# Optimization experiments

Measured on AMD Instinct MI355X. Metric: run time of the kernel, lower is better.

## Reference

```python
import jax, jax.numpy as jnp
import numpy as np

NUM_HEADS = 4
NUM_LEVELS = 4
NUM_POINTS = 8
EMBED = 256
HEAD_DIM = EMBED // NUM_HEADS
SHAPES = np.array([[92, 160], [46, 80], [23, 40], [12, 20]], dtype=np.int64)  # (h, w) per level
NUM_VALUE = int((SHAPES[:, 0] * SHAPES[:, 1]).sum())  # 19560
DEPTH = 64
NQ = 20000
BS = 1
NZ = 4  # num_Z_anchors; NUM_POINTS % NZ == 0


def _depth_bias():
    # replicates init_smpl_off_weights for sampling_offsets_depth.bias
    th = np.arange(NUM_HEADS) * (2.0 * np.pi / NUM_HEADS)
    g = ((np.cos(th) + np.sin(th)) / 2.0)[:, None, None] * np.ones((NUM_HEADS, NUM_LEVELS, NUM_POINTS))
    g = g * (np.arange(NUM_POINTS) + 1)[None, None, :]
    return jnp.asarray(g.reshape(-1), dtype=jnp.float32)


def setup_inputs() -> dict:
    key = jax.random.key(0)
    ks = jax.random.split(key, 8)
    f = jnp.float32
    s = 0.02
    query = jax.random.normal(ks[0], (BS, NQ, EMBED), f)
    value = jax.random.normal(ks[1], (BS, NUM_VALUE, EMBED), f)
    value_dpt_dist = jax.nn.softmax(jax.random.normal(ks[2], (BS, NUM_VALUE, DEPTH), f), axis=-1)
    reference_points = jax.random.uniform(ks[3], (BS, NQ, NZ, 3), f)
    spatial_shapes = jnp.asarray(SHAPES)
    level_start_index = jnp.asarray(np.concatenate([[0], np.cumsum(SHAPES[:, 0] * SHAPES[:, 1])[:-1]]))
    Wv = jax.random.normal(ks[4], (EMBED, EMBED), f) * s
    bv = jnp.zeros((EMBED,), f)
    Wo = jax.random.normal(ks[5], (EMBED, NUM_HEADS * NUM_LEVELS * NUM_POINTS * 2), f) * s
    bo = jax.random.normal(ks[6], (NUM_HEADS * NUM_LEVELS * NUM_POINTS * 2,), f) * 0.5
    Wod = jnp.zeros((EMBED, NUM_HEADS * NUM_LEVELS * NUM_POINTS), f)  # constant_init 0.0
    bod = _depth_bias()
    Wa = jax.random.normal(ks[7], (EMBED, NUM_HEADS * NUM_LEVELS * NUM_POINTS), f) * s
    ba = jnp.zeros((NUM_HEADS * NUM_LEVELS * NUM_POINTS,), f)
    return dict(query=query, value=value, value_dpt_dist=value_dpt_dist,
                reference_points=reference_points, spatial_shapes=spatial_shapes,
                level_start_index=level_start_index, Wv=Wv, bv=bv, Wo=Wo, bo=bo,
                Wod=Wod, bod=bod, Wa=Wa, ba=ba)


def _forward(query, value, value_dpt_dist, reference_points, spatial_shapes,
             level_start_index, Wv, bv, Wo, bo, Wod, bod, Wa, ba):
    bs, nq, _ = query.shape
    H, L, P = NUM_HEADS, NUM_LEVELS, NUM_POINTS
    dh = HEAD_DIM
    D = value_dpt_dist.shape[-1]
    dt = query.dtype
    shapes = np.asarray(spatial_shapes)  # static level shapes

    v = (value @ Wv + bv).reshape(bs, -1, H, dh)  # value_proj
    off_uv = (query @ Wo + bo).reshape(bs, nq, H, L, P, 2)
    off_d = (query @ Wod + bod).reshape(bs, nq, H, L, P, 1)
    off = jnp.concatenate([off_uv, off_d], axis=-1)  # (bs,nq,H,L,P,3)
    attn = jax.nn.softmax((query @ Wa + ba).reshape(bs, nq, H, L * P), axis=-1)
    attn = attn.reshape(bs, nq, H, L, P)

    # offset_normalizer = (w, h, D) per level
    norm = jnp.asarray(np.stack([shapes[:, 1], shapes[:, 0], np.full(L, D)], -1), dtype=dt)
    off = off / norm[None, None, None, :, None, :]
    Z = reference_points.shape[2]
    off = off.reshape(bs, nq, H, L, P // Z, Z, 3)
    loc = (reference_points[:, :, None, None, None, :, :] + off).reshape(bs, nq, H, L, P, 3)

    starts = np.concatenate([[0], np.cumsum(shapes[:, 0] * shapes[:, 1])]).astype(int)
    gather_bh = jax.vmap(jax.vmap(lambda a, i: a[i]))   # over (bs, heads)
    gather_b = jax.vmap(lambda a, i: a[i])              # over bs

    out = jnp.zeros((bs, nq, H, dh), dt)
    for l in range(L):
        Hl, Wl = int(shapes[l, 0]), int(shapes[l, 1])
        v_l = v[:, starts[l]:starts[l + 1]].transpose(0, 2, 1, 3)          # (bs,H,HW,dh)
        d_l = value_dpt_dist[:, starts[l]:starts[l + 1]].reshape(bs, Hl * Wl * D)
        ll = loc[:, :, :, l]                                               # (bs,nq,H,P,3)
        # grid_sample (align_corners=False) pixel coordinates
        x = ll[..., 0] * Wl - 0.5
        y = ll[..., 1] * Hl - 0.5
        z = ll[..., 2] * D - 0.5
        x0f, y0f, z0f = jnp.floor(x), jnp.floor(y), jnp.floor(z)
        fx, fy, fz = x - x0f, y - y0f, z - z0f
        x0 = x0f.astype(jnp.int32); y0 = y0f.astype(jnp.int32); z0 = z0f.astype(jnp.int32)
        z0c = jnp.clip(z0, 0, D - 1)
        z1c = jnp.clip(z0 + 1, 0, D - 1)
        wz0 = (1.0 - fz) * ((z0 >= 0) & (z0 <= D - 1)).astype(dt)
        wz1 = fz * ((z0 + 1 >= 0) & (z0 + 1 <= D - 1)).astype(dt)

        acc = jnp.zeros((bs, nq, H, P, dh), dt)
        for xi, wx in ((x0, 1.0 - fx), (x0 + 1, fx)):
            for yi, wy in ((y0, 1.0 - fy), (y0 + 1, fy)):
                valid = ((xi >= 0) & (xi < Wl) & (yi >= 0) & (yi < Hl)).astype(dt)
                w_uv = wx * wy * valid                                     # (bs,nq,H,P)
                idx = jnp.clip(yi, 0, Hl - 1) * Wl + jnp.clip(xi, 0, Wl - 1)
                idx_h = idx.transpose(0, 2, 1, 3).reshape(bs, H, nq * P)
                val = gather_bh(v_l, idx_h).reshape(bs, H, nq, P, dh).transpose(0, 2, 1, 3, 4)
                d0 = gather_b(d_l, (idx * D + z0c).reshape(bs, -1)).reshape(bs, nq, H, P)
                d1 = gather_b(d_l, (idx * D + z1c).reshape(bs, -1)).reshape(bs, nq, H, P)
                dscore = wz0 * d0 + wz1 * d1                               # depth lerp at this spatial corner
                acc = acc + (w_uv * dscore)[..., None] * val
        out = out + jnp.einsum('bqhp,bqhpd->bqhd', attn[:, :, :, l], acc)
    return out.reshape(bs, nq, H * dh)


def reference(query, value, value_dpt_dist, reference_points, spatial_shapes,
              level_start_index, Wv, bv, Wo, bo, Wod, bod, Wa, ba):
    return _forward(query, value, value_dpt_dist, reference_points, spatial_shapes,
                    level_start_index, Wv, bv, Wo, bo, Wod, bod, Wa, ba)
```

## Files before the change

kernel.cpp:

```cpp
#include <hip/hip_runtime.h>
#include <math.h>

#define NQ    20000
#define NV    19560
#define NHEAD 4
#define DEPTHD 64

typedef __attribute__((ext_vector_type(8))) short short8;
typedef __attribute__((ext_vector_type(4))) float f32x4;

__device__ __forceinline__ ushort f2bf(float f) {
    uint32_t u = __float_as_uint(f);
    uint32_t r = (u + 0x7FFFu + ((u >> 16) & 1u)) >> 16;
    return (ushort)r;
}
__device__ __forceinline__ float bf_lo(uint32_t d) { return __uint_as_float(d << 16); }
__device__ __forceinline__ float bf_hi(uint32_t d) { return __uint_as_float(d & 0xFFFF0000u); }

__global__ __launch_bounds__(256) void prep_weights(
    const float* __restrict__ Wv, const float* __restrict__ Wo,
    const float* __restrict__ Wod, const float* __restrict__ Wa,
    const float* __restrict__ bo, const float* __restrict__ bod,
    const float* __restrict__ ba,
    ushort* __restrict__ WvT, ushort* __restrict__ WqT, float* __restrict__ bq)
{
    const int b = blockIdx.x;
    const int k = threadIdx.x;
    if (b < 256) {
        WvT[b * 256 + k] = f2bf(Wv[k * 256 + b]);
    } else if (b < 768) {
        const int n = b - 256;
        float w;
        if (n < 256)      w = Wo [k * 256 + n];
        else if (n < 384) w = Wod[k * 128 + (n - 256)];
        else              w = Wa [k * 128 + (n - 384)];
        WqT[n * 256 + k] = f2bf(w);
    } else {
        for (int i = k; i < 512; i += 256) {
            float v;
            if (i < 256)      v = bo[i];
            else if (i < 384) v = bod[i - 256];
            else              v = ba[i - 384];
            bq[i] = v;
        }
    }
}

__global__ __launch_bounds__(256) void prep_ddist(
    const float* __restrict__ ddist, uint32_t* __restrict__ ddist2)
{
    const int idx = blockIdx.x * 256 + threadIdx.x;
    if (idx >= NV * 64) return;
    const int z = idx & 63;
    const float lo = ddist[idx];
    const float hi = ddist[idx + ((z < 63) ? 1 : 0)];
    ddist2[idx] = (uint32_t)f2bf(lo) | ((uint32_t)f2bf(hi) << 16);
}

template<bool BF16_OUT>
__global__ __launch_bounds__(256) void gemm_mfma_bf16(
    const float* __restrict__ A, const ushort* __restrict__ BT,
    const float* __restrict__ bias, void* __restrict__ Cout,
    int M, int ldc)
{
    constexpr int K = 256, BK = 32;
    __shared__ ushort Asb[128][40];
    __shared__ ushort Bsb[128][40];

    const int tid  = threadIdx.x;
    const int lane = tid & 63;
    const int wave = tid >> 6;
    const int wm   = wave >> 1;
    const int wn   = wave & 1;
    const int brow = blockIdx.y * 128;
    const int bcol = blockIdx.x * 128;
    const int l15  = lane & 15;
    const int kg   = lane >> 4;

    f32x4 acc[4][4] = {};

    const int rA    = tid >> 1;
    const int partA = tid & 1;

    for (int k0 = 0; k0 < K; k0 += BK) {
        {
            ushort tmp[16];
            if (brow + rA < M) {
                const float* ap = A + (size_t)(brow + rA) * K + k0 + partA * 16;
                #pragma unroll
                for (int i = 0; i < 4; ++i) {
                    float4 v = *reinterpret_cast<const float4*>(ap + i * 4);
                    tmp[i * 4 + 0] = f2bf(v.x);
                    tmp[i * 4 + 1] = f2bf(v.y);
                    tmp[i * 4 + 2] = f2bf(v.z);
                    tmp[i * 4 + 3] = f2bf(v.w);
                }
            } else {
                #pragma unroll
                for (int i = 0; i < 16; ++i) tmp[i] = 0;
            }
            *reinterpret_cast<uint4*>(&Asb[rA][partA * 16 + 0]) = *reinterpret_cast<uint4*>(tmp);
            *reinterpret_cast<uint4*>(&Asb[rA][partA * 16 + 8]) = *reinterpret_cast<uint4*>(tmp + 8);
        }
        #pragma unroll
        for (int i = 0; i < 2; ++i) {
            int f  = tid + i * 256;
            int n  = f >> 2;
            int c8 = (f & 3) * 8;
            uint4 v = *reinterpret_cast<const uint4*>(BT + (size_t)(bcol + n) * K + k0 + c8);
            *reinterpret_cast<uint4*>(&Bsb[n][c8]) = v;
        }
        __syncthreads();

        short8 af[4], bfv[4];
        #pragma unroll
        for (int mf = 0; mf < 4; ++mf)
            af[mf] = *reinterpret_cast<const short8*>(&Asb[wm * 64 + mf * 16 + l15][kg * 8]);
        #pragma unroll
        for (int nf = 0; nf < 4; ++nf)
            bfv[nf] = *reinterpret_cast<const short8*>(&Bsb[wn * 64 + nf * 16 + l15][kg * 8]);
        #pragma unroll
        for (int mf = 0; mf < 4; ++mf)
            #pragma unroll
            for (int nf = 0; nf < 4; ++nf)
                acc[mf][nf] = __builtin_amdgcn_mfma_f32_16x16x32_bf16(af[mf], bfv[nf], acc[mf][nf], 0, 0, 0);
        __syncthreads();
    }

    #pragma unroll
    for (int mf = 0; mf < 4; ++mf) {
        #pragma unroll
        for (int reg = 0; reg < 4; ++reg) {
            int row = brow + wm * 64 + mf * 16 + kg * 4 + reg;
            if (row >= M) continue;
            #pragma unroll
            for (int nf = 0; nf < 4; ++nf) {
                int col = bcol + wn * 64 + nf * 16 + l15;
                float v = acc[mf][nf][reg] + bias[col];
                if (BF16_OUT)
                    ((ushort*)Cout)[(size_t)row * ldc + col] = f2bf(v);
                else
                    ((float*)Cout)[(size_t)row * ldc + col] = v;
            }
        }
    }
}

__global__ __launch_bounds__(256) void deform_sample(
    const float* __restrict__ qproj,
    const ushort* __restrict__ vproj,
    const uint32_t* __restrict__ ddist2,
    const float* __restrict__ refpts,
    float* __restrict__ out)
{
    const int b    = blockIdx.x;
    const int h    = threadIdx.x >> 6;
    const int lane = threadIdx.x & 63;
    const int j    = lane & 31;
    const int qq   = lane >> 5;
    const int q    = 2 * b + qq;

    __shared__ float2 sm[NHEAD][2][128];

    const float* qrow = qproj + (size_t)q * 512;

    float logit = qrow[384 + h * 32 + j];
    float m = logit;
    #pragma unroll
    for (int o = 16; o; o >>= 1) m = fmaxf(m, __shfl_xor(m, o));
    float e = __expf(logit - m);
    float s = e;
    #pragma unroll
    for (int o = 16; o; o >>= 1) s += __shfl_xor(s, o);
    const float aw = e / s;

    const int l  = j >> 3;
    const int p  = j & 7;
    const int zi = p & 3;
    const int Wl = 160 >> l;
    const int Hl = (l == 0) ? 92 : (l == 1) ? 46 : (l == 2) ? 23 : 12;
    const int st = (l == 0) ? 0  : (l == 1) ? 14720 : (l == 2) ? 18400 : 19320;

    const int oidx = (h * 4 + l) * 8 + p;
    const float ox = qrow[oidx * 2 + 0];
    const float oy = qrow[oidx * 2 + 1];
    const float od = qrow[256 + oidx];
    const float rx = refpts[(q * 4 + zi) * 3 + 0];
    const float ry = refpts[(q * 4 + zi) * 3 + 1];
    const float rz = refpts[(q * 4 + zi) * 3 + 2];

    const float x = fmaf(rx, (float)Wl, ox - 0.5f);
    const float y = fmaf(ry, (float)Hl, oy - 0.5f);
    const float z = fmaf(rz, 64.0f,     od - 0.5f);
    const float x0f = floorf(x), y0f = floorf(y), z0f = floorf(z);
    const float fx = x - x0f, fy = y - y0f, fz = z - z0f;
    const int x0 = (int)x0f, y0 = (int)y0f, z0 = (int)z0f;

    const int z0c = min(max(z0, 0), DEPTHD - 1);
    const float wlo = (z0 >= 0 && z0 <= 63) ? (1.f - fz) : ((z0 == -1) ? fz : 0.f);
    const float whi = (z0 >= 0 && z0 <= 62) ? fz : 0.f;

    #pragma unroll
    for (int c = 0; c < 4; ++c) {
        const int   cy = c >> 1, cx = c & 1;
        const int   yi = y0 + cy, xi = x0 + cx;
        const float wy = cy ? fy : (1.f - fy);
        const float wx = cx ? fx : (1.f - fx);
        const bool  valid = (xi >= 0) & (xi < Wl) & (yi >= 0) & (yi < Hl);
        const int   yc = min(max(yi, 0), Hl - 1);
        const int   xc = min(max(xi, 0), Wl - 1);
        const int   row = st + yc * Wl + xc;
        const uint32_t pd = ddist2[row * 64 + z0c];
        const float dscore = wlo * bf_lo(pd) + whi * bf_hi(pd);
        const float coef = valid ? (aw * wx * wy * dscore) : 0.f;
        sm[h][qq][c * 32 + j] = make_float2(coef, __int_as_float(row * 512 + h * 128));
    }

    const int g   = lane >> 3;
    const int ch8 = (lane & 7) << 3;
    const uint32_t chb = (uint32_t)(ch8 << 1);
    const char* vb = (const char*)vproj;
    const float2* s0 = sm[h][0];
    const float2* s1 = sm[h][1];

    float acc0[8] = {}, acc1[8] = {};
    #pragma unroll
    for (int t = 0; t < 16; ++t) {
        const float2 w0 = s0[t * 8 + g];
        const float2 w1 = s1[t * 8 + g];
        const uint4 r0 = *reinterpret_cast<const uint4*>(vb + ((uint32_t)__float_as_int(w0.y) + chb));
        const uint4 r1 = *reinterpret_cast<const uint4*>(vb + ((uint32_t)__float_as_int(w1.y) + chb));
        acc0[0] = fmaf(w0.x, bf_lo(r0.x), acc0[0]);
        acc0[1] = fmaf(w0.x, bf_hi(r0.x), acc0[1]);
        acc0[2] = fmaf(w0.x, bf_lo(r0.y), acc0[2]);
        acc0[3] = fmaf(w0.x, bf_hi(r0.y), acc0[3]);
        acc0[4] = fmaf(w0.x, bf_lo(r0.z), acc0[4]);
        acc0[5] = fmaf(w0.x, bf_hi(r0.z), acc0[5]);
        acc0[6] = fmaf(w0.x, bf_lo(r0.w), acc0[6]);
        acc0[7] = fmaf(w0.x, bf_hi(r0.w), acc0[7]);
        acc1[0] = fmaf(w1.x, bf_lo(r1.x), acc1[0]);
        acc1[1] = fmaf(w1.x, bf_hi(r1.x), acc1[1]);
        acc1[2] = fmaf(w1.x, bf_lo(r1.y), acc1[2]);
        acc1[3] = fmaf(w1.x, bf_hi(r1.y), acc1[3]);
        acc1[4] = fmaf(w1.x, bf_lo(r1.z), acc1[4]);
        acc1[5] = fmaf(w1.x, bf_hi(r1.z), acc1[5]);
        acc1[6] = fmaf(w1.x, bf_lo(r1.w), acc1[6]);
        acc1[7] = fmaf(w1.x, bf_hi(r1.w), acc1[7]);
    }

    #pragma unroll
    for (int o = 8; o <= 32; o <<= 1) {
        #pragma unroll
        for (int k = 0; k < 8; ++k) {
            acc0[k] += __shfl_xor(acc0[k], o);
            acc1[k] += __shfl_xor(acc1[k], o);
        }
    }

    if (g == 0) {
        float* op0 = out + (size_t)(2 * b) * 256 + h * 64 + ch8;
        *reinterpret_cast<float4*>(op0)     = make_float4(acc0[0], acc0[1], acc0[2], acc0[3]);
        *reinterpret_cast<float4*>(op0 + 4) = make_float4(acc0[4], acc0[5], acc0[6], acc0[7]);
        float* op1 = op0 + 256;
        *reinterpret_cast<float4*>(op1)     = make_float4(acc1[0], acc1[1], acc1[2], acc1[3]);
        *reinterpret_cast<float4*>(op1 + 4) = make_float4(acc1[4], acc1[5], acc1[6], acc1[7]);
    }
}

extern "C" void kernel_launch(void* const* d_in, const int* in_sizes, int n_in,
                              void* d_out, int out_size, void* d_ws, size_t ws_size,
                              hipStream_t stream)
{
    const float* query  = (const float*)d_in[0];
    const float* value  = (const float*)d_in[1];
    const float* ddist  = (const float*)d_in[2];
    const float* refpts = (const float*)d_in[3];
    const float* Wv  = (const float*)d_in[6];
    const float* bv  = (const float*)d_in[7];
    const float* Wo  = (const float*)d_in[8];
    const float* bo  = (const float*)d_in[9];
    const float* Wod = (const float*)d_in[10];
    const float* bod = (const float*)d_in[11];
    const float* Wa  = (const float*)d_in[12];
    const float* ba  = (const float*)d_in[13];
    float* out = (float*)d_out;

    char* ws = (char*)d_ws;
    ushort*   vbuf   = (ushort*)ws;
    float*    qbuf   = (float*)(ws + 10014720);
    ushort*   WvT    = (ushort*)(ws + 10014720 + 40960000);
    ushort*   WqT    = WvT + 256 * 256;
    float*    bq     = (float*)(WqT + 512 * 256);
    uint32_t* ddist2 = (uint32_t*)((char*)bq + 2048);

    dim3 blk(256);

    prep_weights<<<dim3(769), blk, 0, stream>>>(Wv, Wo, Wod, Wa, bo, bod, ba, WvT, WqT, bq);
    prep_ddist<<<dim3((NV * 64 + 255) / 256), blk, 0, stream>>>(ddist, ddist2);

    gemm_mfma_bf16<true><<<dim3(2, (NV + 127) / 128), blk, 0, stream>>>(
        value, WvT, bv, vbuf, NV, 256);

    gemm_mfma_bf16<false><<<dim3(4, (NQ + 127) / 128), blk, 0, stream>>>(
        query, WqT, bq, qbuf, NQ, 512);

    deform_sample<<<dim3(NQ / 2), blk, 0, stream>>>(qbuf, vbuf, ddist2, refpts, out);
}
```

Baseline: 156.6 us.

## Merge prep kernels, pre-convert GEMM inputs to bf16, fuse GEMMs, transpose depth table

Merges all preprocessing into one launch. That launch also converts query and value to bf16 up front, so the GEMM loads bf16 A tiles directly instead of converting fp32 in its inner loop. The two projection GEMMs become one launch indexed by grid z, and the depth-distribution table is stored z-major, so the sampling kernel reads a depth plane indexed by spatial row. This cuts launch count and in-loop conversion work but adds an extra write and read of bf16 copies of query and value. It also launches wasted early-exit blocks for the value GEMM.

Result: slower. 167.7 us (+7.1%).

```diff
diff --git a/kernel.cpp b/kernel.cpp
--- a/kernel.cpp
+++ b/kernel.cpp
@@ -17,55 +17,83 @@
 __device__ __forceinline__ float bf_lo(uint32_t d) { return __uint_as_float(d << 16); }
 __device__ __forceinline__ float bf_hi(uint32_t d) { return __uint_as_float(d & 0xFFFF0000u); }
 
-__global__ __launch_bounds__(256) void prep_weights(
+#define PB_WVT0   0
+#define PB_WQT0   256
+#define PB_BIAS   768
+#define PB_DD0    769
+#define PB_DD1    (769 + 4890)
+#define PB_QA1    (PB_DD1 + 2500)
+#define PB_VA1    (PB_QA1 + 2445)
+
+__global__ __launch_bounds__(256) void prep_all(
     const float* __restrict__ Wv, const float* __restrict__ Wo,
     const float* __restrict__ Wod, const float* __restrict__ Wa,
     const float* __restrict__ bo, const float* __restrict__ bod,
-    const float* __restrict__ ba,
-    ushort* __restrict__ WvT, ushort* __restrict__ WqT, float* __restrict__ bq)
+    const float* __restrict__ ba, const float* __restrict__ ddist,
+    const float* __restrict__ query, const float* __restrict__ value,
+    ushort* __restrict__ WvT, ushort* __restrict__ WqT, float* __restrict__ bq,
+    uint32_t* __restrict__ ddist2T, ushort* __restrict__ qA, ushort* __restrict__ vA)
 {
     const int b = blockIdx.x;
-    const int k = threadIdx.x;
-    if (b < 256) {
-        WvT[b * 256 + k] = f2bf(Wv[k * 256 + b]);
-    } else if (b < 768) {
-        const int n = b - 256;
+    const int t = threadIdx.x;
+    if (b < PB_WQT0) {
+        WvT[b * 256 + t] = f2bf(Wv[t * 256 + b]);
+    } else if (b < PB_BIAS) {
+        const int n = b - PB_WQT0;
         float w;
-        if (n < 256)      w = Wo [k * 256 + n];
-        else if (n < 384) w = Wod[k * 128 + (n - 256)];
-        else              w = Wa [k * 128 + (n - 384)];
-        WqT[n * 256 + k] = f2bf(w);
-    } else {
-        for (int i = k; i < 512; i += 256) {
+        if (n < 256)      w = Wo [t * 256 + n];
+        else if (n < 384) w = Wod[t * 128 + (n - 256)];
+        else              w = Wa [t * 128 + (n - 384)];
+        WqT[n * 256 + t] = f2bf(w);
+    } else if (b == PB_BIAS) {
+        for (int i = t; i < 512; i += 256) {
             float v;
             if (i < 256)      v = bo[i];
             else if (i < 384) v = bod[i - 256];
             else              v = ba[i - 384];
             bq[i] = v;
         }
-    }
-}
-
-__global__ __launch_bounds__(256) void prep_ddist(
-    const float* __restrict__ ddist, uint32_t* __restrict__ ddist2)
-{
-    const int idx = blockIdx.x * 256 + threadIdx.x;
-    if (idx >= NV * 64) return;
-    const int z = idx & 63;
-    const float lo = ddist[idx];
-    const float hi = ddist[idx + ((z < 63) ? 1 : 0)];
-    ddist2[idx] = (uint32_t)f2bf(lo) | ((uint32_t)f2bf(hi) << 16);
-}
-
-template<bool BF16_OUT>
-__global__ __launch_bounds__(256) void gemm_mfma_bf16(
-    const float* __restrict__ A, const ushort* __restrict__ BT,
-    const float* __restrict__ bias, void* __restrict__ Cout,
-    int M, int ldc)
+    } else if (b < PB_DD1) {
+        const int idx = (b - PB_DD0) * 256 + t;
+        const int z   = idx & 63;
+        const int row = idx >> 6;
+        const float lo = ddist[idx];
+        const float hi = ddist[idx + ((z < 63) ? 1 : 0)];
+        ddist2T[(size_t)z * NV + row] = (uint32_t)f2bf(lo) | ((uint32_t)f2bf(hi) << 16);
+    } else if (b < PB_QA1) {
+        const size_t i8 = ((size_t)(b - PB_DD1) * 256 + t) * 8;
+        float4 v0 = *reinterpret_cast<const float4*>(query + i8);
+        float4 v1 = *reinterpret_cast<const float4*>(query + i8 + 4);
+        ushort tmp[8] = {f2bf(v0.x), f2bf(v0.y), f2bf(v0.z), f2bf(v0.w),
+                         f2bf(v1.x), f2bf(v1.y), f2bf(v1.z), f2bf(v1.w)};
+        *reinterpret_cast<uint4*>(qA + i8) = *reinterpret_cast<uint4*>(tmp);
+    } else {
+        const size_t i8 = ((size_t)(b - PB_QA1) * 256 + t) * 8;
+        float4 v0 = *reinterpret_cast<const float4*>(value + i8);
+        float4 v1 = *reinterpret_cast<const float4*>(value + i8 + 4);
+        ushort tmp[8] = {f2bf(v0.x), f2bf(v0.y), f2bf(v0.z), f2bf(v0.w),
+                         f2bf(v1.x), f2bf(v1.y), f2bf(v1.z), f2bf(v1.w)};
+        *reinterpret_cast<uint4*>(vA + i8) = *reinterpret_cast<uint4*>(tmp);
+    }
+}
+
+__global__ __launch_bounds__(256) void gemm_fused(
+    const ushort* __restrict__ Av, const ushort* __restrict__ BTv,
+    const float* __restrict__ biasv, ushort* __restrict__ Cv,
+    const ushort* __restrict__ Aq, const ushort* __restrict__ BTq,
+    const float* __restrict__ biasq, float* __restrict__ Cq)
 {
     constexpr int K = 256, BK = 32;
     __shared__ ushort Asb[128][40];
     __shared__ ushort Bsb[128][40];
+
+    const bool isq = (blockIdx.z == 1);
+    if (!isq && (blockIdx.x >= 2 || blockIdx.y >= 153)) return;
+
+    const ushort* A    = isq ? Aq : Av;
+    const ushort* BT   = isq ? BTq : BTv;
+    const float*  bias = isq ? biasq : biasv;
+    const int     M    = isq ? NQ : NV;
 
     const int tid  = threadIdx.x;
     const int lane = tid & 63;
@@ -79,36 +107,18 @@
 
     f32x4 acc[4][4] = {};
 
-    const int rA    = tid >> 1;
-    const int partA = tid & 1;
-
     for (int k0 = 0; k0 < K; k0 += BK) {
-        {
-            ushort tmp[16];
-            if (brow + rA < M) {
-                const float* ap = A + (size_t)(brow + rA) * K + k0 + partA * 16;
-                #pragma unroll
-                for (int i = 0; i < 4; ++i) {
-                    float4 v = *reinterpret_cast<const float4*>(ap + i * 4);
-                    tmp[i * 4 + 0] = f2bf(v.x);
-                    tmp[i * 4 + 1] = f2bf(v.y);
-                    tmp[i * 4 + 2] = f2bf(v.z);
-                    tmp[i * 4 + 3] = f2bf(v.w);
-                }
-            } else {
-                #pragma unroll
-                for (int i = 0; i < 16; ++i) tmp[i] = 0;
-            }
-            *reinterpret_cast<uint4*>(&Asb[rA][partA * 16 + 0]) = *reinterpret_cast<uint4*>(tmp);
-            *reinterpret_cast<uint4*>(&Asb[rA][partA * 16 + 8]) = *reinterpret_cast<uint4*>(tmp + 8);
-        }
         #pragma unroll
         for (int i = 0; i < 2; ++i) {
             int f  = tid + i * 256;
-            int n  = f >> 2;
+            int r  = f >> 2;
             int c8 = (f & 3) * 8;
-            uint4 v = *reinterpret_cast<const uint4*>(BT + (size_t)(bcol + n) * K + k0 + c8);
-            *reinterpret_cast<uint4*>(&Bsb[n][c8]) = v;
+            uint4 av = make_uint4(0, 0, 0, 0);
+            if (brow + r < M)
+                av = *reinterpret_cast<const uint4*>(A + (size_t)(brow + r) * K + k0 + c8);
+            *reinterpret_cast<uint4*>(&Asb[r][c8]) = av;
+            uint4 bv4 = *reinterpret_cast<const uint4*>(BT + (size_t)(bcol + r) * K + k0 + c8);
+            *reinterpret_cast<uint4*>(&Bsb[r][c8]) = bv4;
         }
         __syncthreads();
 
@@ -137,10 +147,10 @@
             for (int nf = 0; nf < 4; ++nf) {
                 int col = bcol + wn * 64 + nf * 16 + l15;
                 float v = acc[mf][nf][reg] + bias[col];
-                if (BF16_OUT)
-                    ((ushort*)Cout)[(size_t)row * ldc + col] = f2bf(v);
+                if (isq)
+                    Cq[(size_t)row * 512 + col] = v;
                 else
-                    ((float*)Cout)[(size_t)row * ldc + col] = v;
+                    Cv[(size_t)row * 256 + col] = f2bf(v);
             }
         }
     }
@@ -149,7 +159,7 @@
 __global__ __launch_bounds__(256) void deform_sample(
     const float* __restrict__ qproj,
     const ushort* __restrict__ vproj,
-    const uint32_t* __restrict__ ddist2,
+    const uint32_t* __restrict__ ddist2T,
     const float* __restrict__ refpts,
     float* __restrict__ out)
 {
@@ -200,6 +210,8 @@
     const float wlo = (z0 >= 0 && z0 <= 63) ? (1.f - fz) : ((z0 == -1) ? fz : 0.f);
     const float whi = (z0 >= 0 && z0 <= 62) ? fz : 0.f;
 
+    const uint32_t* dplane = ddist2T + (size_t)z0c * NV;
+
     #pragma unroll
     for (int c = 0; c < 4; ++c) {
         const int   cy = c >> 1, cx = c & 1;
@@ -210,7 +222,7 @@
         const int   yc = min(max(yi, 0), Hl - 1);
         const int   xc = min(max(xi, 0), Wl - 1);
         const int   row = st + yc * Wl + xc;
-        const uint32_t pd = ddist2[row * 64 + z0c];
+        const uint32_t pd = dplane[row];
         const float dscore = wlo * bf_lo(pd) + whi * bf_hi(pd);
         const float coef = valid ? (aw * wx * wy * dscore) : 0.f;
         sm[h][qq][c * 32 + j] = make_float2(coef, __int_as_float(row * 512 + h * 128));
@@ -286,23 +298,23 @@
     float* out = (float*)d_out;
 
     char* ws = (char*)d_ws;
-    ushort*   vbuf   = (ushort*)ws;
-    float*    qbuf   = (float*)(ws + 10014720);
-    ushort*   WvT    = (ushort*)(ws + 10014720 + 40960000);
-    ushort*   WqT    = WvT + 256 * 256;
-    float*    bq     = (float*)(WqT + 512 * 256);
-    uint32_t* ddist2 = (uint32_t*)((char*)bq + 2048);
+    ushort*   vbuf    = (ushort*)ws;
+    float*    qbuf    = (float*)(ws + 10014720);
+    ushort*   WvT     = (ushort*)(ws + 10014720 + 40960000);
+    ushort*   WqT     = WvT + 256 * 256;
+    float*    bq      = (float*)(WqT + 512 * 256);
+    uint32_t* ddist2T = (uint32_t*)((char*)bq + 2048);
+    ushort*   qA      = (ushort*)((char*)ddist2T + 5007360);
+    ushort*   vA      = qA + (size_t)NQ * 256;
 
     dim3 blk(256);
 
-    prep_weights<<<dim3(769), blk, 0, stream>>>(Wv, Wo, Wod, Wa, bo, bod, ba, WvT, WqT, bq);
-    prep_ddist<<<dim3((NV * 64 + 255) / 256), blk, 0, stream>>>(ddist, ddist2);
-
-    gemm_mfma_bf16<true><<<dim3(2, (NV + 127) / 128), blk, 0, stream>>>(
-        value, WvT, bv, vbuf, NV, 256);
-
-    gemm_mfma_bf16<false><<<dim3(4, (NQ + 127) / 128), blk, 0, stream>>>(
-        query, WqT, bq, qbuf, NQ, 512);
-
-    deform_sample<<<dim3(NQ / 2), blk, 0, stream>>>(qbuf, vbuf, ddist2, refpts, out);
-}
+    prep_all<<<dim3(PB_VA1), blk, 0, stream>>>(
+        Wv, Wo, Wod, Wa, bo, bod, ba, ddist, query, value,
+        WvT, WqT, bq, ddist2T, qA, vA);
+
+    gemm_fused<<<dim3(4, 157, 2), blk, 0, stream>>>(
+        vA, WvT, bv, vbuf, qA, WqT, bq, qbuf);
+
+    deform_sample<<<dim3(NQ / 2), blk, 0, stream>>>(qbuf, vbuf, ddist2T, refpts, out);
+}
```
